# Performance work log

Hardware: AMD Instinct MI355X
Metric: run time of the kernel (lower is better)

## Reference

```python
import jax, jax.numpy as jnp
import numpy as np
from jax import lax

H = 16        # num_heads
MB = 16       # mini_batch_size
LR = 1.0      # TTT inner learning rate
ROPE_BASE = 10000.0
LN_EPS = 1e-5


def setup_inputs() -> dict:
    key = jax.random.key(0)
    ks = jax.random.split(key, 4)
    B, S, D = 4, 4096, 2048
    x = jax.random.normal(ks[0], (B, S, D), dtype=jnp.float32)
    scale = 1.0 / np.sqrt(D)  # keep projections well-conditioned
    Wk = jax.random.normal(ks[1], (D, D), dtype=jnp.float32) * scale
    Wv = jax.random.normal(ks[2], (D, D), dtype=jnp.float32) * scale
    Wo = jax.random.normal(ks[3], (D, D), dtype=jnp.float32) * scale
    ln_gamma = jnp.ones((D,), dtype=jnp.float32)
    ln_beta = jnp.zeros((D,), dtype=jnp.float32)
    return {"x": x, "Wk": Wk, "Wv": Wv, "Wo": Wo,
            "ln_gamma": ln_gamma, "ln_beta": ln_beta}


def _rotate_half(u):
    u1, u2 = jnp.split(u, 2, axis=-1)
    return jnp.concatenate([-u2, u1], axis=-1)


def reference(x, Wk, Wv, Wo, ln_gamma, ln_beta):
    B, S, Dm = x.shape
    Dh = Dm // H
    # K/V projections (nn.Linear: x @ W^T), split heads -> [B,H,S,Dh]
    k = (x @ Wk.T).reshape(B, S, H, Dh).transpose(0, 2, 1, 3)
    v = (x @ Wv.T).reshape(B, S, H, Dh).transpose(0, 2, 1, 3)

    # RoPE on keys
    inv_freq = 1.0 / ROPE_BASE ** (jnp.arange(0, Dh, 2, dtype=jnp.float32) / Dh)
    t = jnp.arange(S, dtype=jnp.float32)
    freqs = t[:, None] * inv_freq[None, :]          # [S, Dh/2]
    emb = jnp.concatenate([freqs, freqs], axis=-1)  # [S, Dh]
    cos, sin = jnp.cos(emb), jnp.sin(emb)
    k = k * cos + _rotate_half(k) * sin

    # chunk into mini-batches for the TTT scan: [nmb, B, H, MB, Dh]
    nmb = S // MB
    k_c = k.reshape(B, H, nmb, MB, Dh).transpose(2, 0, 1, 3, 4)
    v_c = v.reshape(B, H, nmb, MB, Dh).transpose(2, 0, 1, 3, 4)

    # hidden state: identity per (batch, head)
    W0 = jnp.broadcast_to(jnp.eye(Dh, dtype=x.dtype), (B, H, Dh, Dh))

    inv_n = 2.0 / (MB * Dh)  # grad of mean-MSE over mini-batch elements

    def step(W, kv):
        kc, vc = kv                                   # [B,H,MB,Dh]
        z = jnp.einsum('bhsd,bhde->bhse', kc, W)      # prediction f(k; W)
        grad = jnp.einsum('bhsd,bhse->bhde', kc, (z - vc) * inv_n)
        return W - LR * grad, z

    _, zs = lax.scan(step, W0, (k_c, v_c))            # zs: [nmb,B,H,MB,Dh]
    out = zs.transpose(1, 2, 0, 3, 4).reshape(B, H, S, Dh)
    out = out.transpose(0, 2, 1, 3).reshape(B, S, Dm)

    # LayerNorm then output projection
    mu = jnp.mean(out, axis=-1, keepdims=True)
    var = jnp.var(out, axis=-1, keepdims=True)
    out = (out - mu) * lax.rsqrt(var + LN_EPS) * ln_gamma + ln_beta
    return out @ Wo.T
```

## Files before the change

### kernel.cpp

```cpp
#include <hip/hip_runtime.h>
#include <hip/hip_bf16.h>


typedef __attribute__((ext_vector_type(4)))  float f32x4;
typedef __attribute__((ext_vector_type(16))) float f32x16;
typedef __attribute__((ext_vector_type(8)))  short s16x8;
typedef __attribute__((ext_vector_type(4)))  short s16x4;

#define B_   4
#define S_   4096
#define D_   2048
#define H_   16
#define DH_  128
#define MB_  16
#define NMB_ 256

__device__ __forceinline__ float b2f(short u){
  union { unsigned int i; float f; } x;
  x.i = ((unsigned int)(unsigned short)u) << 16;
  return x.f;
}
__device__ __forceinline__ short f2b(float f){
  __hip_bfloat16 h = __float2bfloat16(f);
  return *reinterpret_cast<short*>(&h);
}
__device__ __forceinline__ void gll16(const void* g, void* l){
  __builtin_amdgcn_global_load_lds(
      (const __attribute__((address_space(1))) unsigned int*)g,
      (__attribute__((address_space(3))) unsigned int*)l, 16, 0, 0);
}

__global__ __launch_bounds__(256) void cvt_kernel(
    const float* __restrict__ in, unsigned short* __restrict__ out, int n8)
{
  int i = blockIdx.x * 256 + threadIdx.x;
  if (i >= n8) return;
  const float4* p = (const float4*)in + (size_t)i * 2;
  float4 a = p[0], b = p[1];
  s16x8 o;
  o[0] = f2b(a.x); o[1] = f2b(a.y); o[2] = f2b(a.z); o[3] = f2b(a.w);
  o[4] = f2b(b.x); o[5] = f2b(b.y); o[6] = f2b(b.z); o[7] = f2b(b.w);
  *(s16x8*)&out[(size_t)i * 8] = o;
}

__global__ void rope_tab_kernel(float* __restrict__ tab){
  int idx = blockIdx.x * 256 + threadIdx.x;
  if (idx >= S_ * 64) return;
  int s = idx >> 6, i = idx & 63;
  double invf = pow(10000.0, -(double)(2 * i) / 128.0);
  double ang  = (double)s * invf;
  tab[s * 128 + i]      = (float)cos(ang);
  tab[s * 128 + 64 + i] = (float)sin(ang);
}

template<int MODE>
__global__ __launch_bounds__(256) void gemm_kernel(
    const unsigned short* __restrict__ A,
    const unsigned short* __restrict__ W0,
    const unsigned short* __restrict__ W1,
    const float* __restrict__ rope_tab,
    unsigned short* __restrict__ k_out,
    unsigned short* __restrict__ v_out,
    float* __restrict__ f_out)
{
  __shared__ __align__(16) char lds[36864];
  const int tid = threadIdx.x;
  const int w = tid >> 6, l = tid & 63;
  const int bid = blockIdx.x;
  const int tile_m = bid & 127;
  const int tile_n = bid >> 7;

  const unsigned short* Wsel = W0;
  int nrow0 = tile_n * 128;
  if (MODE == 0 && tile_n >= 16){ Wsel = W1; nrow0 = (tile_n - 16) * 128; }

  size_t gA[4], gB[4]; int ldso[4];
  for (int i = 0; i < 4; ++i){
    int q   = tid + i * 256;
    int row = q >> 3;
    int cbl = ((q & 7) * 16) ^ ((row & 7) << 4);
    gA[i]   = (size_t)(tile_m * 128 + row) * (D_ * 2) + cbl;
    gB[i]   = (size_t)(nrow0 + row) * (D_ * 2) + cbl;
    ldso[i] = q * 16;
  }
  const char* Ab = (const char*)A;
  const char* Wb = (const char*)Wsel;

  f32x4 acc[4][4];
  for (int mi = 0; mi < 4; ++mi) for (int ni = 0; ni < 4; ++ni)
    acc[mi][ni] = (f32x4){0.f, 0.f, 0.f, 0.f};

  const int lr = l & 15, lk = l >> 4;
  const int m0 = (w >> 1) * 64, n0 = (w & 1) * 64;

  for (int kt = 0; kt < D_ / 64; ++kt){
    size_t ko = (size_t)kt * 128;
    #pragma unroll
    for (int i = 0; i < 4; ++i) gll16(Ab + gA[i] + ko, &lds[ldso[i]]);
    #pragma unroll
    for (int i = 0; i < 4; ++i) gll16(Wb + gB[i] + ko, &lds[16384 + ldso[i]]);
    __syncthreads();
    #pragma unroll
    for (int ks = 0; ks < 2; ++ks){
      s16x8 af[4], bfr[4];
      #pragma unroll
      for (int mi = 0; mi < 4; ++mi){
        int r = m0 + 16 * mi + lr;
        af[mi] = *(const s16x8*)&lds[r * 128 + ((64 * ks + 16 * lk) ^ ((r & 7) << 4))];
      }
      #pragma unroll
      for (int ni = 0; ni < 4; ++ni){
        int r = n0 + 16 * ni + lr;
        bfr[ni] = *(const s16x8*)&lds[16384 + r * 128 + ((64 * ks + 16 * lk) ^ ((r & 7) << 4))];
      }
      #pragma unroll
      for (int mi = 0; mi < 4; ++mi)
        #pragma unroll
        for (int ni = 0; ni < 4; ++ni)
          acc[mi][ni] = __builtin_amdgcn_mfma_f32_16x16x32_bf16(af[mi], bfr[ni], acc[mi][ni], 0, 0, 0);
    }
    __syncthreads();
  }

  if (MODE == 1){
    #pragma unroll
    for (int mi = 0; mi < 4; ++mi){
      #pragma unroll
      for (int ni = 0; ni < 4; ++ni){
        int col  = n0 + 16 * ni + lr;
        int rowb = m0 + 16 * mi + 4 * lk;
        size_t gbase = ((size_t)tile_m * 128 + rowb) * D_ + (size_t)tile_n * 128 + col;
        #pragma unroll
        for (int r = 0; r < 4; ++r)
          f_out[gbase + (size_t)r * D_] = acc[mi][ni][r];
      }
    }
    return;
  }

  #pragma unroll
  for (int mi = 0; mi < 4; ++mi){
    #pragma unroll
    for (int ni = 0; ni < 4; ++ni){
      int col  = n0 + 16 * ni + lr;
      int rowb = m0 + 16 * mi + 4 * lk;
      #pragma unroll
      for (int r = 0; r < 4; ++r)
        *(unsigned short*)&lds[(rowb + r) * 272 + col * 2] = (unsigned short)f2b(acc[mi][ni][r]);
    }
  }
  __syncthreads();

  const int r    = tid >> 1, half = tid & 1;
  const size_t grow = (size_t)tile_m * 128 + r;
  const int bb = (int)(grow >> 12);
  const int ss = (int)(grow & 4095);
  #pragma unroll
  for (int j = 0; j < 8; ++j){
    int c0 = half * 64 + 8 * j;
    s16x8 vals = *(const s16x8*)&lds[r * 272 + c0 * 2];
    if (tile_n >= 16){
      int h = tile_n - 16;
      *(s16x8*)&v_out[(((size_t)bb * H_ + h) * S_ + ss) * DH_ + c0] = vals;
    } else {
      int h = tile_n;
      s16x8 part = *(const s16x8*)&lds[r * 272 + (c0 ^ 64) * 2];
      int i0 = c0 & 63;
      float sgn = half ? 1.0f : -1.0f;
      s16x8 o;
      #pragma unroll
      for (int e = 0; e < 8; ++e){
        float cs = rope_tab[ss * 128 + i0 + e];
        float sn = rope_tab[ss * 128 + 64 + i0 + e];
        o[e] = f2b(b2f(vals[e]) * cs + sgn * b2f(part[e]) * sn);
      }
      *(s16x8*)&k_out[(((size_t)bb * H_ + h) * S_ + ss) * DH_ + c0] = o;
    }
  }
}

#define WT_OFF  0
#define KC_OFF  16384
#define KCT_OFF 20480
#define VCT_OFF 30720
#define DT_OFF  33280

__global__ __launch_bounds__(256) void ttt_scan(
    const unsigned short* __restrict__ k_scan,
    const unsigned short* __restrict__ v_scan,
    unsigned short* __restrict__ ttt)
{
  __shared__ __align__(16) char lds[38400];
  const int tid = threadIdx.x, l = tid & 63, w = tid >> 6;
  const int blk = blockIdx.x, eh = blk & 1, bh = blk >> 1;
  const int h = bh & 15, b = bh >> 4;
  const int eb = eh * 64;
  const size_t kv_base = (size_t)bh * S_ * DH_;
  const float SCALE_NEG = -2.0f / (MB_ * DH_);

  for (int idx = tid; idx < 64 * 128; idx += 256){
    int e = idx >> 7, d = idx & 127;
    unsigned short val = (d == eb + e) ? (unsigned short)0x3F80 : (unsigned short)0;
    *(unsigned short*)&lds[WT_OFF + e * 256 + ((2 * d) ^ ((e & 7) << 4))] = val;
  }
  const int lc = l & 31, lh5 = l >> 5;
  f32x16 Wf[2];
  #pragma unroll
  for (int n = 0; n < 2; ++n)
    #pragma unroll
    for (int rr = 0; rr < 16; ++rr){
      int d = 32 * w + (rr & 3) + 8 * (rr >> 2) + 4 * lh5;
      int e = 32 * n + lc;
      Wf[n][rr] = (d == eb + e) ? 1.0f : 0.0f;
    }

  const int srow = tid >> 4;
  const int sc16 = tid & 15;
  s16x8 kreg = *(const s16x8*)&k_scan[kv_base + srow * 128 + sc16 * 8];
  s16x4 vreg = *(const s16x4*)&v_scan[kv_base + srow * 128 + eb + sc16 * 4];

  const int lr = l & 15, lk = l >> 4;

  for (int c = 0; c < NMB_; ++c){
    *(s16x8*)&lds[KC_OFF + srow * 256 + ((sc16 * 16) ^ ((srow & 7) << 4))] = kreg;
    #pragma unroll
    for (int j = 0; j < 8; ++j){
      int jp = (j + sc16) & 7;
      *(unsigned short*)&lds[KCT_OFF + (sc16 * 8 + jp) * 80 + srow * 2] = (unsigned short)kreg[jp];
    }
    #pragma unroll
    for (int j = 0; j < 4; ++j){
      int jp = (j + sc16) & 3;
      *(unsigned short*)&lds[VCT_OFF + (sc16 * 4 + jp) * 40 + srow * 2] = (unsigned short)vreg[jp];
    }
    if (c + 1 < NMB_){
      size_t nb = kv_base + (size_t)(c + 1) * (MB_ * DH_);
      kreg = *(const s16x8*)&k_scan[nb + srow * 128 + sc16 * 8];
      vreg = *(const s16x4*)&v_scan[nb + srow * 128 + eb + sc16 * 4];
    }
    __syncthreads();

    f32x4 z = (f32x4){0.f, 0.f, 0.f, 0.f};
    const int ep = 16 * w + lr;
    #pragma unroll
    for (int ks = 0; ks < 4; ++ks){
      s16x8 a  = *(const s16x8*)&lds[KC_OFF + lr * 256 + ((64 * ks + 16 * lk) ^ ((lr & 7) << 4))];
      s16x8 bb2 = *(const s16x8*)&lds[WT_OFF + ep * 256 + ((64 * ks + 16 * lk) ^ ((ep & 7) << 4))];
      z = __builtin_amdgcn_mfma_f32_16x16x32_bf16(a, bb2, z, 0, 0, 0);
    }
    {
      const int s0 = 4 * lk;
      s16x4 vv = *(const s16x4*)&lds[VCT_OFF + ep * 40 + s0 * 2];
      s16x4 dpack;
      size_t orow = ((size_t)b * S_ + c * MB_ + s0) * D_ + h * DH_ + eb + ep;
      #pragma unroll
      for (int rr = 0; rr < 4; ++rr){
        float zv = z[rr];
        ttt[orow + (size_t)rr * D_] = (unsigned short)f2b(zv);
        dpack[rr] = f2b((zv - b2f(vv[rr])) * SCALE_NEG);
      }
      *(s16x4*)&lds[DT_OFF + ep * 80 + s0 * 2] = dpack;
    }
    __syncthreads();

    {
      s16x8 a = *(const s16x8*)&lds[KCT_OFF + (32 * w + lc) * 80 + 16 * lh5];
      #pragma unroll
      for (int n = 0; n < 2; ++n){
        s16x8 bb2 = *(const s16x8*)&lds[DT_OFF + (32 * n + lc) * 80 + 16 * lh5];
        Wf[n] = __builtin_amdgcn_mfma_f32_32x32x16_bf16(a, bb2, Wf[n], 0, 0, 0);
      }
      #pragma unroll
      for (int n = 0; n < 2; ++n){
        int e = 32 * n + lc;
        #pragma unroll
        for (int g = 0; g < 4; ++g){
          int d0 = 32 * w + 8 * g + 4 * lh5;
          s16x4 p;
          #pragma unroll
          for (int rr = 0; rr < 4; ++rr) p[rr] = f2b(Wf[n][4 * g + rr]);
          *(s16x4*)&lds[WT_OFF + e * 256 + ((2 * d0) ^ ((e & 7) << 4))] = p;
        }
      }
    }
    __syncthreads();
  }
}

__global__ __launch_bounds__(256) void ln_kernel(
    unsigned short* __restrict__ io,
    const float* __restrict__ gamma,
    const float* __restrict__ beta)
{
  const int row = blockIdx.x, tid = threadIdx.x;
  const size_t base = (size_t)row * D_ + tid * 8;
  s16x8 v = *(const s16x8*)&io[base];
  float f[8], s1 = 0.f, s2 = 0.f;
  #pragma unroll
  for (int j = 0; j < 8; ++j){ f[j] = b2f(v[j]); s1 += f[j]; s2 += f[j] * f[j]; }
  #pragma unroll
  for (int off = 32; off; off >>= 1){
    s1 += __shfl_xor(s1, off);
    s2 += __shfl_xor(s2, off);
  }
  __shared__ float red[8];
  const int w = tid >> 6, l = tid & 63;
  if (l == 0){ red[w] = s1; red[4 + w] = s2; }
  __syncthreads();
  s1 = red[0] + red[1] + red[2] + red[3];
  s2 = red[4] + red[5] + red[6] + red[7];
  const float mu  = s1 * (1.0f / D_);
  const float var = s2 * (1.0f / D_) - mu * mu;
  const float rs  = rsqrtf(var + 1e-5f);
  const float4* gp = (const float4*)&gamma[tid * 8];
  const float4* bp = (const float4*)&beta[tid * 8];
  float4 g0 = gp[0], g1 = gp[1], b0 = bp[0], b1 = bp[1];
  float gg[8] = {g0.x,g0.y,g0.z,g0.w,g1.x,g1.y,g1.z,g1.w};
  float bb[8] = {b0.x,b0.y,b0.z,b0.w,b1.x,b1.y,b1.z,b1.w};
  s16x8 o;
  #pragma unroll
  for (int j = 0; j < 8; ++j)
    o[j] = f2b((f[j] - mu) * rs * gg[j] + bb[j]);
  *(s16x8*)&io[base] = o;
}

extern "C" void kernel_launch(void* const* d_in, const int* in_sizes, int n_in,
                              void* d_out, int out_size, void* d_ws, size_t ws_size,
                              hipStream_t stream)
{
  const float* x     = (const float*)d_in[0];
  const float* Wk    = (const float*)d_in[1];
  const float* Wv    = (const float*)d_in[2];
  const float* Wo    = (const float*)d_in[3];
  const float* gamma = (const float*)d_in[4];
  const float* beta  = (const float*)d_in[5];
  float* out = (float*)d_out;

  char* ws = (char*)d_ws;
  float* rope_tab        = (float*)ws;
  unsigned short* xb     = (unsigned short*)(ws + (2u << 20));
  unsigned short* k_scan = (unsigned short*)(ws + (2u << 20) + 1 * 67108864ull);
  unsigned short* v_scan = (unsigned short*)(ws + (2u << 20) + 2 * 67108864ull);
  unsigned short* Wkb    = (unsigned short*)(ws + (2u << 20) + 3 * 67108864ull);
  unsigned short* Wvb    = (unsigned short*)(ws + (2u << 20) + 3 * 67108864ull + 1 * 8388608ull);
  unsigned short* Wob    = (unsigned short*)(ws + (2u << 20) + 3 * 67108864ull + 2 * 8388608ull);
  unsigned short* ttt    = xb;

  const int nx8 = B_ * S_ * D_ / 8;
  const int nw8 = D_ * D_ / 8;
  cvt_kernel<<<dim3(nx8 / 256), dim3(256), 0, stream>>>(x,  xb,  nx8);
  cvt_kernel<<<dim3(nw8 / 256), dim3(256), 0, stream>>>(Wk, Wkb, nw8);
  cvt_kernel<<<dim3(nw8 / 256), dim3(256), 0, stream>>>(Wv, Wvb, nw8);
  cvt_kernel<<<dim3(nw8 / 256), dim3(256), 0, stream>>>(Wo, Wob, nw8);
  rope_tab_kernel<<<dim3(1024), dim3(256), 0, stream>>>(rope_tab);

  gemm_kernel<0><<<dim3(128 * 32), dim3(256), 0, stream>>>(
      xb, Wkb, Wvb, rope_tab, k_scan, v_scan, nullptr);
  ttt_scan<<<dim3(128), dim3(256), 0, stream>>>(k_scan, v_scan, ttt);
  ln_kernel<<<dim3(B_ * S_), dim3(256), 0, stream>>>(ttt, gamma, beta);
  gemm_kernel<1><<<dim3(128 * 16), dim3(256), 0, stream>>>(
      ttt, Wob, nullptr, nullptr, nullptr, nullptr, out);
}
```

Before: 1.107 ms.

## Double-buffer TTT scan chunks, remap GEMM tiles, coalesce output stores, fuse weight casts

The TTT scan now double-buffers the k/v chunk staging in LDS. Chunk c+1 is written while chunk c is computed, and global loads run two chunks ahead, which drops one barrier per step. Transpose row pitches change from 80 to 88 bytes, which is meant to reduce bank conflicts. The GEMMs get a block-index remap so that blocks grouped by XCD share A and W tiles, and the output GEMM stages its fp32 results through LDS for coalesced 16-byte stores. The three weight-cast launches are merged into one. The cost is more LDS in the scan, which is fine at one block per CU, plus extra barriers in the output epilogue.

```diff
diff --git a/kernel.cpp b/kernel.cpp
--- a/kernel.cpp
+++ b/kernel.cpp
@@ -43,6 +43,24 @@
   *(s16x8*)&out[(size_t)i * 8] = o;
 }
 
+__global__ __launch_bounds__(256) void cvt3_kernel(
+    const float* __restrict__ w0, const float* __restrict__ w1, const float* __restrict__ w2,
+    unsigned short* __restrict__ o0, unsigned short* __restrict__ o1, unsigned short* __restrict__ o2)
+{
+  const int per = D_ * D_ / 8;
+  int i = blockIdx.x * 256 + threadIdx.x;
+  const float* in; unsigned short* out;
+  if (i < per)            { in = w0; out = o0; }
+  else if (i < 2 * per)   { in = w1; out = o1; i -= per; }
+  else                    { in = w2; out = o2; i -= 2 * per; }
+  const float4* p = (const float4*)in + (size_t)i * 2;
+  float4 a = p[0], b = p[1];
+  s16x8 o;
+  o[0] = f2b(a.x); o[1] = f2b(a.y); o[2] = f2b(a.z); o[3] = f2b(a.w);
+  o[4] = f2b(b.x); o[5] = f2b(b.y); o[6] = f2b(b.z); o[7] = f2b(b.w);
+  *(s16x8*)&out[(size_t)i * 8] = o;
+}
+
 __global__ void rope_tab_kernel(float* __restrict__ tab){
   int idx = blockIdx.x * 256 + threadIdx.x;
   if (idx >= S_ * 64) return;
@@ -53,90 +71,82 @@
   tab[s * 128 + 64 + i] = (float)sin(ang);
 }
 
-template<int MODE>
-__global__ __launch_bounds__(256) void gemm_kernel(
+__device__ __forceinline__ void mainloop_128(
+    const char* __restrict__ Ab, const char* __restrict__ Wb,
+    char* lds, int tid, f32x4 (&acc)[4][4])
+{
+  const int w = tid >> 6, l = tid & 63;
+  const int lr = l & 15, lk = l >> 4;
+  const int m0 = (w >> 1) * 64, n0 = (w & 1) * 64;
+
+  size_t g[4]; int ldso[4];
+  #pragma unroll
+  for (int i = 0; i < 4; ++i){
+    int q   = tid + i * 256;
+    int row = q >> 3;
+    int cbl = ((q & 7) * 16) ^ ((row & 7) << 4);
+    g[i]    = (size_t)row * (D_ * 2) + cbl;
+    ldso[i] = q * 16;
+  }
+
+  for (int kt = 0; kt < D_ / 64; ++kt){
+    size_t ko = (size_t)kt * 128;
+    #pragma unroll
+    for (int i = 0; i < 4; ++i) gll16(Ab + g[i] + ko, &lds[ldso[i]]);
+    #pragma unroll
+    for (int i = 0; i < 4; ++i) gll16(Wb + g[i] + ko, &lds[16384 + ldso[i]]);
+    __syncthreads();
+    #pragma unroll
+    for (int ks = 0; ks < 2; ++ks){
+      s16x8 af[4], bfr[4];
+      #pragma unroll
+      for (int mi = 0; mi < 4; ++mi){
+        int r = m0 + 16 * mi + lr;
+        af[mi] = *(const s16x8*)&lds[r * 128 + ((64 * ks + 16 * lk) ^ ((r & 7) << 4))];
+      }
+      #pragma unroll
+      for (int ni = 0; ni < 4; ++ni){
+        int r = n0 + 16 * ni + lr;
+        bfr[ni] = *(const s16x8*)&lds[16384 + r * 128 + ((64 * ks + 16 * lk) ^ ((r & 7) << 4))];
+      }
+      #pragma unroll
+      for (int mi = 0; mi < 4; ++mi)
+        #pragma unroll
+        for (int ni = 0; ni < 4; ++ni)
+          acc[mi][ni] = __builtin_amdgcn_mfma_f32_16x16x32_bf16(af[mi], bfr[ni], acc[mi][ni], 0, 0, 0);
+    }
+    __syncthreads();
+  }
+}
+
+__global__ __launch_bounds__(256) void gemm_kv(
     const unsigned short* __restrict__ A,
     const unsigned short* __restrict__ W0,
     const unsigned short* __restrict__ W1,
     const float* __restrict__ rope_tab,
     unsigned short* __restrict__ k_out,
-    unsigned short* __restrict__ v_out,
-    float* __restrict__ f_out)
+    unsigned short* __restrict__ v_out)
 {
   __shared__ __align__(16) char lds[36864];
   const int tid = threadIdx.x;
-  const int w = tid >> 6, l = tid & 63;
   const int bid = blockIdx.x;
-  const int tile_m = bid & 127;
-  const int tile_n = bid >> 7;
-
-  const unsigned short* Wsel = W0;
-  int nrow0 = tile_n * 128;
-  if (MODE == 0 && tile_n >= 16){ Wsel = W1; nrow0 = (tile_n - 16) * 128; }
-
-  size_t gA[4], gB[4]; int ldso[4];
-  for (int i = 0; i < 4; ++i){
-    int q   = tid + i * 256;
-    int row = q >> 3;
-    int cbl = ((q & 7) * 16) ^ ((row & 7) << 4);
-    gA[i]   = (size_t)(tile_m * 128 + row) * (D_ * 2) + cbl;
-    gB[i]   = (size_t)(nrow0 + row) * (D_ * 2) + cbl;
-    ldso[i] = q * 16;
-  }
-  const char* Ab = (const char*)A;
-  const char* Wb = (const char*)Wsel;
+  const int local  = bid >> 3;
+  const int tile_n = (bid & 7) * 4 + (local & 3);
+  const int tile_m = local >> 2;
+
+  const unsigned short* Wsel = (tile_n >= 16) ? W1 : W0;
+  const int nrow0 = (tile_n >= 16) ? (tile_n - 16) * 128 : tile_n * 128;
 
   f32x4 acc[4][4];
   for (int mi = 0; mi < 4; ++mi) for (int ni = 0; ni < 4; ++ni)
     acc[mi][ni] = (f32x4){0.f, 0.f, 0.f, 0.f};
 
+  mainloop_128((const char*)A + (size_t)tile_m * 128 * (D_ * 2),
+               (const char*)Wsel + (size_t)nrow0 * (D_ * 2), lds, tid, acc);
+
+  const int w = tid >> 6, l = tid & 63;
   const int lr = l & 15, lk = l >> 4;
   const int m0 = (w >> 1) * 64, n0 = (w & 1) * 64;
-
-  for (int kt = 0; kt < D_ / 64; ++kt){
-    size_t ko = (size_t)kt * 128;
-    #pragma unroll
-    for (int i = 0; i < 4; ++i) gll16(Ab + gA[i] + ko, &lds[ldso[i]]);
-    #pragma unroll
-    for (int i = 0; i < 4; ++i) gll16(Wb + gB[i] + ko, &lds[16384 + ldso[i]]);
-    __syncthreads();
-    #pragma unroll
-    for (int ks = 0; ks < 2; ++ks){
-      s16x8 af[4], bfr[4];
-      #pragma unroll
-      for (int mi = 0; mi < 4; ++mi){
-        int r = m0 + 16 * mi + lr;
-        af[mi] = *(const s16x8*)&lds[r * 128 + ((64 * ks + 16 * lk) ^ ((r & 7) << 4))];
-      }
-      #pragma unroll
-      for (int ni = 0; ni < 4; ++ni){
-        int r = n0 + 16 * ni + lr;
-        bfr[ni] = *(const s16x8*)&lds[16384 + r * 128 + ((64 * ks + 16 * lk) ^ ((r & 7) << 4))];
-      }
-      #pragma unroll
-      for (int mi = 0; mi < 4; ++mi)
-        #pragma unroll
-        for (int ni = 0; ni < 4; ++ni)
-          acc[mi][ni] = __builtin_amdgcn_mfma_f32_16x16x32_bf16(af[mi], bfr[ni], acc[mi][ni], 0, 0, 0);
-    }
-    __syncthreads();
-  }
-
-  if (MODE == 1){
-    #pragma unroll
-    for (int mi = 0; mi < 4; ++mi){
-      #pragma unroll
-      for (int ni = 0; ni < 4; ++ni){
-        int col  = n0 + 16 * ni + lr;
-        int rowb = m0 + 16 * mi + 4 * lk;
-        size_t gbase = ((size_t)tile_m * 128 + rowb) * D_ + (size_t)tile_n * 128 + col;
-        #pragma unroll
-        for (int r = 0; r < 4; ++r)
-          f_out[gbase + (size_t)r * D_] = acc[mi][ni][r];
-      }
-    }
-    return;
-  }
 
   #pragma unroll
   for (int mi = 0; mi < 4; ++mi){
@@ -179,18 +189,90 @@
   }
 }
 
+__global__ __launch_bounds__(256) void gemm_out(
+    const unsigned short* __restrict__ A,
+    const unsigned short* __restrict__ W0,
+    float* __restrict__ f_out)
+{
+  __shared__ __align__(16) char lds[36864];
+  const int tid = threadIdx.x;
+  const int bid = blockIdx.x;
+  const int local  = bid >> 3;
+  const int tile_n = (bid & 7) * 2 + (local & 1);
+  const int tile_m = local >> 1;
+
+  f32x4 acc[4][4];
+  for (int mi = 0; mi < 4; ++mi) for (int ni = 0; ni < 4; ++ni)
+    acc[mi][ni] = (f32x4){0.f, 0.f, 0.f, 0.f};
+
+  mainloop_128((const char*)A + (size_t)tile_m * 128 * (D_ * 2),
+               (const char*)W0 + (size_t)tile_n * 128 * (D_ * 2), lds, tid, acc);
+
+  const int w = tid >> 6, l = tid & 63;
+  const int lr = l & 15, lk = l >> 4;
+  const int n0 = (w & 1) * 64;
+  const int mh_own = w >> 1;
+  float* lf = (float*)lds;
+
+  #pragma unroll
+  for (int mh = 0; mh < 2; ++mh){
+    __syncthreads();
+    if (mh_own == mh){
+      #pragma unroll
+      for (int mi = 0; mi < 4; ++mi){
+        #pragma unroll
+        for (int ni = 0; ni < 4; ++ni){
+          int col = n0 + 16 * ni + lr;
+          int rowl = 16 * mi + 4 * lk;
+          #pragma unroll
+          for (int r = 0; r < 4; ++r)
+            lf[(rowl + r) * 132 + col] = acc[mi][ni][r];
+        }
+      }
+    }
+    __syncthreads();
+    #pragma unroll
+    for (int j2 = 0; j2 < 8; ++j2){
+      int idx = tid + 256 * j2;
+      int row = idx >> 5, c4 = idx & 31;
+      f32x4 vv = *(const f32x4*)&lf[row * 132 + c4 * 4];
+      size_t grow = (size_t)tile_m * 128 + mh * 64 + row;
+      *(f32x4*)&f_out[grow * D_ + (size_t)tile_n * 128 + c4 * 4] = vv;
+    }
+  }
+}
+
 #define WT_OFF  0
 #define KC_OFF  16384
-#define KCT_OFF 20480
-#define VCT_OFF 30720
-#define DT_OFF  33280
+#define KCT_OFF 24576
+#define VCT_OFF 47104
+#define DT_OFF  52224
+
+__device__ __forceinline__ void stage_chunk(char* lds, int buf, int srow, int sc16,
+                                            const s16x8& kreg, const s16x4& vreg)
+{
+  char* kc  = lds + KC_OFF  + buf * 4096;
+  char* kct = lds + KCT_OFF + buf * 11264;
+  char* vct = lds + VCT_OFF + buf * 2560;
+  *(s16x8*)&kc[srow * 256 + ((sc16 * 16) ^ ((srow & 7) << 4))] = kreg;
+  #pragma unroll
+  for (int j = 0; j < 8; ++j){
+    int jp = (j + sc16) & 7;
+    *(unsigned short*)&kct[(sc16 * 8 + jp) * 88 + srow * 2] = (unsigned short)kreg[jp];
+  }
+  #pragma unroll
+  for (int j = 0; j < 4; ++j){
+    int jp = (j + sc16) & 3;
+    *(unsigned short*)&vct[(sc16 * 4 + jp) * 40 + srow * 2] = (unsigned short)vreg[jp];
+  }
+}
 
 __global__ __launch_bounds__(256) void ttt_scan(
     const unsigned short* __restrict__ k_scan,
     const unsigned short* __restrict__ v_scan,
     unsigned short* __restrict__ ttt)
 {
-  __shared__ __align__(16) char lds[38400];
+  __shared__ __align__(16) char lds[57856];
   const int tid = threadIdx.x, l = tid & 63, w = tid >> 6;
   const int blk = blockIdx.x, eh = blk & 1, bh = blk >> 1;
   const int h = bh & 15, b = bh >> 4;
@@ -218,39 +300,38 @@
   const int sc16 = tid & 15;
   s16x8 kreg = *(const s16x8*)&k_scan[kv_base + srow * 128 + sc16 * 8];
   s16x4 vreg = *(const s16x4*)&v_scan[kv_base + srow * 128 + eb + sc16 * 4];
+  stage_chunk(lds, 0, srow, sc16, kreg, vreg);
+  {
+    size_t nb = kv_base + (size_t)(MB_ * DH_);
+    kreg = *(const s16x8*)&k_scan[nb + srow * 128 + sc16 * 8];
+    vreg = *(const s16x4*)&v_scan[nb + srow * 128 + eb + sc16 * 4];
+  }
+  __syncthreads();
 
   const int lr = l & 15, lk = l >> 4;
 
   for (int c = 0; c < NMB_; ++c){
-    *(s16x8*)&lds[KC_OFF + srow * 256 + ((sc16 * 16) ^ ((srow & 7) << 4))] = kreg;
-    #pragma unroll
-    for (int j = 0; j < 8; ++j){
-      int jp = (j + sc16) & 7;
-      *(unsigned short*)&lds[KCT_OFF + (sc16 * 8 + jp) * 80 + srow * 2] = (unsigned short)kreg[jp];
-    }
-    #pragma unroll
-    for (int j = 0; j < 4; ++j){
-      int jp = (j + sc16) & 3;
-      *(unsigned short*)&lds[VCT_OFF + (sc16 * 4 + jp) * 40 + srow * 2] = (unsigned short)vreg[jp];
-    }
-    if (c + 1 < NMB_){
-      size_t nb = kv_base + (size_t)(c + 1) * (MB_ * DH_);
+    const int cur = c & 1;
+    if (c + 1 < NMB_) stage_chunk(lds, cur ^ 1, srow, sc16, kreg, vreg);
+    if (c + 2 < NMB_){
+      size_t nb = kv_base + (size_t)(c + 2) * (MB_ * DH_);
       kreg = *(const s16x8*)&k_scan[nb + srow * 128 + sc16 * 8];
       vreg = *(const s16x4*)&v_scan[nb + srow * 128 + eb + sc16 * 4];
     }
-    __syncthreads();
-
+
+    const char* kc = lds + KC_OFF + cur * 4096;
     f32x4 z = (f32x4){0.f, 0.f, 0.f, 0.f};
     const int ep = 16 * w + lr;
     #pragma unroll
     for (int ks = 0; ks < 4; ++ks){
-      s16x8 a  = *(const s16x8*)&lds[KC_OFF + lr * 256 + ((64 * ks + 16 * lk) ^ ((lr & 7) << 4))];
+      s16x8 a   = *(const s16x8*)&kc[lr * 256 + ((64 * ks + 16 * lk) ^ ((lr & 7) << 4))];
       s16x8 bb2 = *(const s16x8*)&lds[WT_OFF + ep * 256 + ((64 * ks + 16 * lk) ^ ((ep & 7) << 4))];
       z = __builtin_amdgcn_mfma_f32_16x16x32_bf16(a, bb2, z, 0, 0, 0);
     }
     {
+      const char* vct = lds + VCT_OFF + cur * 2560;
       const int s0 = 4 * lk;
-      s16x4 vv = *(const s16x4*)&lds[VCT_OFF + ep * 40 + s0 * 2];
+      s16x4 vv = *(const s16x4*)&vct[ep * 40 + s0 * 2];
       s16x4 dpack;
       size_t orow = ((size_t)b * S_ + c * MB_ + s0) * D_ + h * DH_ + eb + ep;
       #pragma unroll
@@ -259,15 +340,16 @@
         ttt[orow + (size_t)rr * D_] = (unsigned short)f2b(zv);
         dpack[rr] = f2b((zv - b2f(vv[rr])) * SCALE_NEG);
       }
-      *(s16x4*)&lds[DT_OFF + ep * 80 + s0 * 2] = dpack;
+      *(s16x4*)&lds[DT_OFF + ep * 88 + s0 * 2] = dpack;
     }
     __syncthreads();
 
     {
-      s16x8 a = *(const s16x8*)&lds[KCT_OFF + (32 * w + lc) * 80 + 16 * lh5];
+      const char* kct = lds + KCT_OFF + cur * 11264;
+      s16x8 a = *(const s16x8*)&kct[(32 * w + lc) * 88 + 16 * lh5];
       #pragma unroll
       for (int n = 0; n < 2; ++n){
-        s16x8 bb2 = *(const s16x8*)&lds[DT_OFF + (32 * n + lc) * 80 + 16 * lh5];
+        s16x8 bb2 = *(const s16x8*)&lds[DT_OFF + (32 * n + lc) * 88 + 16 * lh5];
         Wf[n] = __builtin_amdgcn_mfma_f32_32x32x16_bf16(a, bb2, Wf[n], 0, 0, 0);
       }
       #pragma unroll
@@ -348,16 +430,12 @@
 
   const int nx8 = B_ * S_ * D_ / 8;
   const int nw8 = D_ * D_ / 8;
-  cvt_kernel<<<dim3(nx8 / 256), dim3(256), 0, stream>>>(x,  xb,  nx8);
-  cvt_kernel<<<dim3(nw8 / 256), dim3(256), 0, stream>>>(Wk, Wkb, nw8);
-  cvt_kernel<<<dim3(nw8 / 256), dim3(256), 0, stream>>>(Wv, Wvb, nw8);
-  cvt_kernel<<<dim3(nw8 / 256), dim3(256), 0, stream>>>(Wo, Wob, nw8);
+  cvt_kernel<<<dim3(nx8 / 256), dim3(256), 0, stream>>>(x, xb, nx8);
+  cvt3_kernel<<<dim3(3 * nw8 / 256), dim3(256), 0, stream>>>(Wk, Wv, Wo, Wkb, Wvb, Wob);
   rope_tab_kernel<<<dim3(1024), dim3(256), 0, stream>>>(rope_tab);
 
-  gemm_kernel<0><<<dim3(128 * 32), dim3(256), 0, stream>>>(
-      xb, Wkb, Wvb, rope_tab, k_scan, v_scan, nullptr);
+  gemm_kv<<<dim3(4096), dim3(256), 0, stream>>>(xb, Wkb, Wvb, rope_tab, k_scan, v_scan);
   ttt_scan<<<dim3(128), dim3(256), 0, stream>>>(k_scan, v_scan, ttt);
   ln_kernel<<<dim3(B_ * S_), dim3(256), 0, stream>>>(ttt, gamma, beta);
-  gemm_kernel<1><<<dim3(128 * 16), dim3(256), 0, stream>>>(
-      ttt, Wob, nullptr, nullptr, nullptr, nullptr, out);
-}
+  gemm_out<<<dim3(2048), dim3(256), 0, stream>>>(ttt, Wob, out);
+}
```

Result: faster. 1.079 ms (-2.6%).
